# Optimization experiments

Measured on AMD Instinct MI355X. Metric: run time of the kernel, lower is better.

The kernel has to match this reference:

```python
import jax, jax.numpy as jnp
from jax import lax
import numpy as np

DECAY = 0.9
THRESH = 1.0


def setup_inputs() -> dict:
    key = jax.random.key(0)
    k1, k2, k3 = jax.random.split(key, 3)
    B, T, I, H, O = 64, 256, 1024, 2048, 1024
    x = jax.random.normal(k1, (B, T, I), dtype=jnp.float32)
    W1 = jax.random.normal(k2, (I, H), dtype=jnp.float32) * (1.0 / np.sqrt(I))
    b1 = jnp.zeros((H,), dtype=jnp.float32)
    W2 = jax.random.normal(k3, (H, O), dtype=jnp.float32) * (1.0 / np.sqrt(H))
    b2 = jnp.zeros((O,), dtype=jnp.float32)
    return {"x": x, "W1": W1, "b1": b1, "W2": W2, "b2": b2}


def reference(x, W1, b1, W2, b2):
    B, T, I = x.shape
    H = W1.shape[1]
    # Batch fc1 across all timesteps in one GEMM: [B,T,H]
    cur = jnp.einsum('bti,ih->bth', x, W1) + b1
    cur_tm = jnp.swapaxes(cur, 0, 1)  # [T,B,H] time-major for scan

    def step(carry, cur_t):
        mem, _ = carry
        mem = mem * DECAY + cur_t * (1.0 - DECAY)
        fired = mem > THRESH
        spk = jnp.where(fired, 1.0, 0.0).astype(mem.dtype)
        mem = jnp.where(fired, 0.0, mem)
        return (mem, spk), None

    mem0 = jnp.zeros((B, H), dtype=x.dtype)
    spk0 = jnp.zeros((B, H), dtype=x.dtype)
    (_, spk_last), _ = lax.scan(step, (mem0, spk0), cur_tm)
    # fc2 applied only to the final spike pattern, as in the original
    return spk_last @ W2 + b2
```

## Files before the change

### kernel.cpp

```cpp
#include <hip/hip_runtime.h>


typedef __attribute__((ext_vector_type(16))) float f32x16;
typedef __attribute__((ext_vector_type(8))) short s16x8;

#define GPTR(p) ((const __attribute__((address_space(1))) void*)(p))
#define SPTR(p) ((__attribute__((address_space(3))) void*)(p))

static constexpr int Bsz = 64, Tsz = 256, Isz = 1024, Hsz = 2048, Osz = 1024;
static constexpr int BK = 16;
static constexpr int NKT = Isz / BK;
static constexpr int NB = 128;
static constexpr int AL_OFF = 4096, B_OFF = 8192;
static constexpr int BUFEL = 12288;
static constexpr int ST = 68;
static constexpr int LDS_USHORTS = 3 * BUFEL;

__device__ __forceinline__ unsigned short f2bf(float f) {
  unsigned u = __float_as_uint(f);
  u += 0x7FFFu + ((u >> 16) & 1u);
  return (unsigned short)(u >> 16);
}
__device__ __forceinline__ float bf2f(unsigned short h) {
  return __uint_as_float(((unsigned)h) << 16);
}

__global__ void split_x_kernel(const float* __restrict__ x,
                               unsigned short* __restrict__ hi,
                               unsigned short* __restrict__ lo) {
  const long i = (long)blockIdx.x * 256 + threadIdx.x;
  const float4 v = ((const float4*)x)[i];
  const unsigned short hx = f2bf(v.x), hy = f2bf(v.y), hz = f2bf(v.z), hw = f2bf(v.w);
  ushort4 H, L;
  H.x = hx; H.y = hy; H.z = hz; H.w = hw;
  L.x = f2bf(v.x - bf2f(hx));
  L.y = f2bf(v.y - bf2f(hy));
  L.z = f2bf(v.z - bf2f(hz));
  L.w = f2bf(v.w - bf2f(hw));
  ((ushort4*)hi)[i] = H;
  ((ushort4*)lo)[i] = L;
}

__global__ void w1_transpose_split_kernel(const float* __restrict__ W1,
                                          unsigned short* __restrict__ wh,
                                          unsigned short* __restrict__ wl) {
  __shared__ float tile[32][33];
  const int h0 = blockIdx.x * 32;
  const int i0 = blockIdx.y * 32;
  const int c = threadIdx.x & 31;
  const int r4 = threadIdx.x >> 5;
#pragma unroll
  for (int s = 0; s < 4; ++s) {
    const int r = r4 + s * 8;
    tile[r][c] = W1[(long)(i0 + r) * Hsz + h0 + c];
  }
  __syncthreads();
#pragma unroll
  for (int s = 0; s < 4; ++s) {
    const int hr = r4 + s * 8;
    const float v = tile[c][hr];
    const unsigned short hh = f2bf(v);
    wh[(long)(h0 + hr) * Isz + i0 + c] = hh;
    wl[(long)(h0 + hr) * Isz + i0 + c] = f2bf(v - bf2f(hh));
  }
}

__global__ __launch_bounds__(512, 4) void gemm1_scan_kernel(
    const unsigned short* __restrict__ xh, const unsigned short* __restrict__ xl,
    const unsigned short* __restrict__ wth, const unsigned short* __restrict__ wtl,
    const float* __restrict__ b1, float* __restrict__ spk) {
  __shared__ __align__(16) unsigned short lds[LDS_USHORTS];

  const int tid = threadIdx.x;
  const int l = tid & 63;
  const int w = tid >> 6;
  const int wm = w >> 1;
  const int wn = w & 1;
  const int b = blockIdx.y;
  const int hb = blockIdx.x * NB;

  const int arow = tid >> 1;
  const int brow = (tid >> 1) & 127;
  const int ch8 = (tid & 1) * 8;
  const unsigned short* gAh = xh + (long)(b * Tsz + arow) * Isz + ch8;
  const unsigned short* gAl = xl + (long)(b * Tsz + arow) * Isz + ch8;
  const unsigned short* gB = ((tid < 256) ? wth : wtl) + (long)(hb + brow) * Isz + ch8;

#define STG(Q, KT) do {                                                                   \
    unsigned short* d_ = lds + (Q) * BUFEL + tid * 8;                                     \
    __builtin_amdgcn_global_load_lds(GPTR(gAh + (long)(KT) * BK), SPTR(d_), 16, 0, 0);    \
    __builtin_amdgcn_global_load_lds(GPTR(gAl + (long)(KT) * BK), SPTR(d_ + AL_OFF), 16, 0, 0); \
    __builtin_amdgcn_global_load_lds(GPTR(gB + (long)(KT) * BK), SPTR(d_ + B_OFF), 16, 0, 0);   \
  } while (0)

  const int lr = l & 31;
  const int kc = (l >> 5) * 8;
  const int aoff0 = (wm * 64 + lr) * 16 + kc;
  const int boff0 = B_OFF + (wn * 64 + lr) * 16 + kc;

  f32x16 acc[2][2];
#pragma unroll
  for (int i = 0; i < 2; ++i)
#pragma unroll
    for (int j = 0; j < 2; ++j) acc[i][j] = (f32x16)(0.f);

#define MM(MI, NI, AF, BF) \
  acc[MI][NI] = __builtin_amdgcn_mfma_f32_32x32x16_bf16(AF, BF, acc[MI][NI], 0, 0, 0)

  STG(0, 0);
  STG(1, 1);
  asm volatile("s_waitcnt vmcnt(3)" ::: "memory");
  __builtin_amdgcn_s_barrier();

  for (int kt = 0; kt < NKT; ++kt) {
    const int q = kt % 3;
    const unsigned short* p = lds + q * BUFEL;

    if (kt + 2 < NKT) {
      const int qn = (q >= 1) ? q - 1 : 2;
      STG(qn, kt + 2);
    }

    s16x8 Ah0 = *(const s16x8*)(p + aoff0);
    s16x8 Ah1 = *(const s16x8*)(p + aoff0 + 512);
    s16x8 Al0 = *(const s16x8*)(p + AL_OFF + aoff0);
    s16x8 Al1 = *(const s16x8*)(p + AL_OFF + aoff0 + 512);
    s16x8 Bh0 = *(const s16x8*)(p + boff0);
    s16x8 Bh1 = *(const s16x8*)(p + boff0 + 512);
    s16x8 Bl0 = *(const s16x8*)(p + boff0 + 2048);
    s16x8 Bl1 = *(const s16x8*)(p + boff0 + 2048 + 512);

    MM(0, 0, Ah0, Bh0); MM(0, 1, Ah0, Bh1);
    MM(1, 0, Ah1, Bh0); MM(1, 1, Ah1, Bh1);
    MM(0, 0, Ah0, Bl0); MM(0, 1, Ah0, Bl1);
    MM(1, 0, Ah1, Bl0); MM(1, 1, Ah1, Bl1);
    MM(0, 0, Al0, Bh0); MM(0, 1, Al0, Bh1);
    MM(1, 0, Al1, Bh0); MM(1, 1, Al1, Bh1);

    if (kt < NKT - 2) asm volatile("s_waitcnt vmcnt(3)" ::: "memory");
    else              asm volatile("s_waitcnt vmcnt(0)" ::: "memory");
    __builtin_amdgcn_s_barrier();
  }

  __syncthreads();
  float* scanbuf = reinterpret_cast<float*>(lds);
  float memv = 0.f;
  int fired = 0;
  const float b1v = (tid < NB) ? b1[hb + tid] : 0.f;

  for (int rnd = 0; rnd < 4; ++rnd) {
    if (wm == rnd) {
#pragma unroll
      for (int mi = 0; mi < 2; ++mi)
#pragma unroll
        for (int ni = 0; ni < 2; ++ni) {
          const int col = wn * 64 + ni * 32 + lr;
          float* dst = scanbuf + col * ST + mi * 32 + 4 * (l >> 5);
#pragma unroll
          for (int rq = 0; rq < 4; ++rq) {
            float4 v;
            v.x = acc[mi][ni][rq * 4 + 0];
            v.y = acc[mi][ni][rq * 4 + 1];
            v.z = acc[mi][ni][rq * 4 + 2];
            v.w = acc[mi][ni][rq * 4 + 3];
            *reinterpret_cast<float4*>(dst + 8 * rq) = v;
          }
        }
    }
    __syncthreads();
    if (tid < NB) {
      const float* src = scanbuf + tid * ST;
      float4 cur = *reinterpret_cast<const float4*>(src);
      for (int t0 = 0; t0 < 64; t0 += 4) {
        const int tn = (t0 + 4 < 64) ? t0 + 4 : t0;
        const float4 nxt = *reinterpret_cast<const float4*>(src + tn);
        float c;
        c = cur.x + b1v; memv = memv * 0.9f + c * 0.1f; fired = memv > 1.0f; if (fired) memv = 0.f;
        c = cur.y + b1v; memv = memv * 0.9f + c * 0.1f; fired = memv > 1.0f; if (fired) memv = 0.f;
        c = cur.z + b1v; memv = memv * 0.9f + c * 0.1f; fired = memv > 1.0f; if (fired) memv = 0.f;
        c = cur.w + b1v; memv = memv * 0.9f + c * 0.1f; fired = memv > 1.0f; if (fired) memv = 0.f;
        cur = nxt;
      }
    }
    __syncthreads();
  }
  if (tid < NB) spk[(long)b * Hsz + hb + tid] = fired ? 1.0f : 0.0f;
}

__global__ void gemm2_kernel(const float* __restrict__ spk, const float* __restrict__ W2,
                             const float* __restrict__ b2, float* __restrict__ out) {
  __shared__ int s_cnt[256];
  __shared__ int s_off[257];
  __shared__ int s_list[Hsz];
  const int b = blockIdx.x;
  const int tid = threadIdx.x;
  int hs[8];
  int c = 0;
#pragma unroll
  for (int e = 0; e < 8; ++e) {
    const int h = tid * 8 + e;
    if (spk[(long)b * Hsz + h] > 0.5f) hs[c++] = h;
  }
  s_cnt[tid] = c;
  __syncthreads();
  if (tid == 0) {
    int s = 0;
    for (int i = 0; i < 256; ++i) { s_off[i] = s; s += s_cnt[i]; }
    s_off[256] = s;
  }
  __syncthreads();
  {
    const int base = s_off[tid];
    for (int i = 0; i < c; ++i) s_list[base + i] = hs[i];
  }
  __syncthreads();
  const int total = s_off[256];
#pragma unroll
  for (int q = 0; q < 4; ++q) {
    const int o = q * 256 + tid;
    float v = b2[o];
    for (int i = 0; i < total; ++i) v += W2[(long)s_list[i] * Osz + o];
    out[(long)b * Osz + o] = v;
  }
}

extern "C" void kernel_launch(void* const* d_in, const int* in_sizes, int n_in,
                              void* d_out, int out_size, void* d_ws, size_t ws_size,
                              hipStream_t stream) {
  const float* x = (const float*)d_in[0];
  const float* W1 = (const float*)d_in[1];
  const float* b1 = (const float*)d_in[2];
  const float* W2 = (const float*)d_in[3];
  const float* b2 = (const float*)d_in[4];
  float* out = (float*)d_out;

  unsigned short* xh = (unsigned short*)d_ws;
  unsigned short* xl = xh + (long)Bsz * Tsz * Isz;
  unsigned short* wh = xl + (long)Bsz * Tsz * Isz;
  unsigned short* wl = wh + (long)Hsz * Isz;
  float* spk = (float*)(wl + (long)Hsz * Isz);

  split_x_kernel<<<(Bsz * Tsz * Isz) / (256 * 4), 256, 0, stream>>>(x, xh, xl);
  w1_transpose_split_kernel<<<dim3(Hsz / 32, Isz / 32), 256, 0, stream>>>(W1, wh, wl);
  gemm1_scan_kernel<<<dim3(Hsz / NB, Bsz), 512, 0, stream>>>(xh, xl, wh, wl, b1, spk);
  gemm2_kernel<<<Bsz, 256, 0, stream>>>(spk, W2, b2, out);
}
```

Measured before the change: 252.1 us.

## Enlarge per-wave GEMM tile to 128x64 with 256-thread blocks

Halves the block to 4 waves and gives each wave a 128x64 output tile (4x2 MFMA accumulators) instead of 64x64. Each B fragment read from LDS now feeds twice as many MFMAs, which cuts LDS read traffic per flop. Staging issues six global-to-LDS loads per thread to cover the same tile, and the wait counts are adjusted to match. The scan now runs in two rounds of 128 timesteps with a wider row stride. The price is more accumulator registers per wave and fewer resident waves to hide latency.

```diff
diff --git a/kernel.cpp b/kernel.cpp
--- a/kernel.cpp
+++ b/kernel.cpp
@@ -11,9 +11,9 @@
 static constexpr int BK = 16;
 static constexpr int NKT = Isz / BK;
 static constexpr int NB = 128;
-static constexpr int AL_OFF = 4096, B_OFF = 8192;
+static constexpr int AL_OFF = 4096, BH_OFF = 8192, BL_OFF = 10240;
 static constexpr int BUFEL = 12288;
-static constexpr int ST = 68;
+static constexpr int ST = 132;
 static constexpr int LDS_USHORTS = 3 * BUFEL;
 
 __device__ __forceinline__ unsigned short f2bf(float f) {
@@ -65,7 +65,7 @@
   }
 }
 
-__global__ __launch_bounds__(512, 4) void gemm1_scan_kernel(
+__global__ __launch_bounds__(256, 2) void gemm1_scan_kernel(
     const unsigned short* __restrict__ xh, const unsigned short* __restrict__ xl,
     const unsigned short* __restrict__ wth, const unsigned short* __restrict__ wtl,
     const float* __restrict__ b1, float* __restrict__ spk) {
@@ -79,28 +79,31 @@
   const int b = blockIdx.y;
   const int hb = blockIdx.x * NB;
 
-  const int arow = tid >> 1;
-  const int brow = (tid >> 1) & 127;
+  const int srow = tid >> 1;
   const int ch8 = (tid & 1) * 8;
-  const unsigned short* gAh = xh + (long)(b * Tsz + arow) * Isz + ch8;
-  const unsigned short* gAl = xl + (long)(b * Tsz + arow) * Isz + ch8;
-  const unsigned short* gB = ((tid < 256) ? wth : wtl) + (long)(hb + brow) * Isz + ch8;
+  const unsigned short* gAh = xh + (long)(b * Tsz + srow) * Isz + ch8;
+  const unsigned short* gAl = xl + (long)(b * Tsz + srow) * Isz + ch8;
+  const unsigned short* gBh = wth + (long)(hb + srow) * Isz + ch8;
+  const unsigned short* gBl = wtl + (long)(hb + srow) * Isz + ch8;
 
 #define STG(Q, KT) do {                                                                   \
     unsigned short* d_ = lds + (Q) * BUFEL + tid * 8;                                     \
     __builtin_amdgcn_global_load_lds(GPTR(gAh + (long)(KT) * BK), SPTR(d_), 16, 0, 0);    \
-    __builtin_amdgcn_global_load_lds(GPTR(gAl + (long)(KT) * BK), SPTR(d_ + AL_OFF), 16, 0, 0); \
-    __builtin_amdgcn_global_load_lds(GPTR(gB + (long)(KT) * BK), SPTR(d_ + B_OFF), 16, 0, 0);   \
+    __builtin_amdgcn_global_load_lds(GPTR(gAh + 128 * Isz + (long)(KT) * BK), SPTR(d_ + 2048), 16, 0, 0); \
+    __builtin_amdgcn_global_load_lds(GPTR(gAl + (long)(KT) * BK), SPTR(d_ + AL_OFF), 16, 0, 0);           \
+    __builtin_amdgcn_global_load_lds(GPTR(gAl + 128 * Isz + (long)(KT) * BK), SPTR(d_ + AL_OFF + 2048), 16, 0, 0); \
+    __builtin_amdgcn_global_load_lds(GPTR(gBh + (long)(KT) * BK), SPTR(d_ + BH_OFF), 16, 0, 0);           \
+    __builtin_amdgcn_global_load_lds(GPTR(gBl + (long)(KT) * BK), SPTR(d_ + BL_OFF), 16, 0, 0);           \
   } while (0)
 
   const int lr = l & 31;
   const int kc = (l >> 5) * 8;
-  const int aoff0 = (wm * 64 + lr) * 16 + kc;
-  const int boff0 = B_OFF + (wn * 64 + lr) * 16 + kc;
-
-  f32x16 acc[2][2];
-#pragma unroll
-  for (int i = 0; i < 2; ++i)
+  const int aoff = (wm * 128 + lr) * 16 + kc;
+  const int boff = BH_OFF + (wn * 64 + lr) * 16 + kc;
+
+  f32x16 acc[4][2];
+#pragma unroll
+  for (int i = 0; i < 4; ++i)
 #pragma unroll
     for (int j = 0; j < 2; ++j) acc[i][j] = (f32x16)(0.f);
 
@@ -109,7 +112,7 @@
 
   STG(0, 0);
   STG(1, 1);
-  asm volatile("s_waitcnt vmcnt(3)" ::: "memory");
+  asm volatile("s_waitcnt vmcnt(6)" ::: "memory");
   __builtin_amdgcn_s_barrier();
 
   for (int kt = 0; kt < NKT; ++kt) {
@@ -121,23 +124,33 @@
       STG(qn, kt + 2);
     }
 
-    s16x8 Ah0 = *(const s16x8*)(p + aoff0);
-    s16x8 Ah1 = *(const s16x8*)(p + aoff0 + 512);
-    s16x8 Al0 = *(const s16x8*)(p + AL_OFF + aoff0);
-    s16x8 Al1 = *(const s16x8*)(p + AL_OFF + aoff0 + 512);
-    s16x8 Bh0 = *(const s16x8*)(p + boff0);
-    s16x8 Bh1 = *(const s16x8*)(p + boff0 + 512);
-    s16x8 Bl0 = *(const s16x8*)(p + boff0 + 2048);
-    s16x8 Bl1 = *(const s16x8*)(p + boff0 + 2048 + 512);
+    s16x8 Ah0 = *(const s16x8*)(p + aoff);
+    s16x8 Ah1 = *(const s16x8*)(p + aoff + 512);
+    s16x8 Ah2 = *(const s16x8*)(p + aoff + 1024);
+    s16x8 Ah3 = *(const s16x8*)(p + aoff + 1536);
+    s16x8 Al0 = *(const s16x8*)(p + AL_OFF + aoff);
+    s16x8 Al1 = *(const s16x8*)(p + AL_OFF + aoff + 512);
+    s16x8 Al2 = *(const s16x8*)(p + AL_OFF + aoff + 1024);
+    s16x8 Al3 = *(const s16x8*)(p + AL_OFF + aoff + 1536);
+    s16x8 Bh0 = *(const s16x8*)(p + boff);
+    s16x8 Bh1 = *(const s16x8*)(p + boff + 512);
+    s16x8 Bl0 = *(const s16x8*)(p + boff + 2048);
+    s16x8 Bl1 = *(const s16x8*)(p + boff + 2048 + 512);
 
     MM(0, 0, Ah0, Bh0); MM(0, 1, Ah0, Bh1);
     MM(1, 0, Ah1, Bh0); MM(1, 1, Ah1, Bh1);
+    MM(2, 0, Ah2, Bh0); MM(2, 1, Ah2, Bh1);
+    MM(3, 0, Ah3, Bh0); MM(3, 1, Ah3, Bh1);
     MM(0, 0, Ah0, Bl0); MM(0, 1, Ah0, Bl1);
     MM(1, 0, Ah1, Bl0); MM(1, 1, Ah1, Bl1);
+    MM(2, 0, Ah2, Bl0); MM(2, 1, Ah2, Bl1);
+    MM(3, 0, Ah3, Bl0); MM(3, 1, Ah3, Bl1);
     MM(0, 0, Al0, Bh0); MM(0, 1, Al0, Bh1);
     MM(1, 0, Al1, Bh0); MM(1, 1, Al1, Bh1);
-
-    if (kt < NKT - 2) asm volatile("s_waitcnt vmcnt(3)" ::: "memory");
+    MM(2, 0, Al2, Bh0); MM(2, 1, Al2, Bh1);
+    MM(3, 0, Al3, Bh0); MM(3, 1, Al3, Bh1);
+
+    if (kt < NKT - 2) asm volatile("s_waitcnt vmcnt(6)" ::: "memory");
     else              asm volatile("s_waitcnt vmcnt(0)" ::: "memory");
     __builtin_amdgcn_s_barrier();
   }
@@ -148,10 +161,10 @@
   int fired = 0;
   const float b1v = (tid < NB) ? b1[hb + tid] : 0.f;
 
-  for (int rnd = 0; rnd < 4; ++rnd) {
+  for (int rnd = 0; rnd < 2; ++rnd) {
     if (wm == rnd) {
 #pragma unroll
-      for (int mi = 0; mi < 2; ++mi)
+      for (int mi = 0; mi < 4; ++mi)
 #pragma unroll
         for (int ni = 0; ni < 2; ++ni) {
           const int col = wn * 64 + ni * 32 + lr;
@@ -171,8 +184,8 @@
     if (tid < NB) {
       const float* src = scanbuf + tid * ST;
       float4 cur = *reinterpret_cast<const float4*>(src);
-      for (int t0 = 0; t0 < 64; t0 += 4) {
-        const int tn = (t0 + 4 < 64) ? t0 + 4 : t0;
+      for (int t0 = 0; t0 < 128; t0 += 4) {
+        const int tn = (t0 + 4 < 128) ? t0 + 4 : t0;
         const float4 nxt = *reinterpret_cast<const float4*>(src + tn);
         float c;
         c = cur.x + b1v; memv = memv * 0.9f + c * 0.1f; fired = memv > 1.0f; if (fired) memv = 0.f;
@@ -242,6 +255,6 @@
 
   split_x_kernel<<<(Bsz * Tsz * Isz) / (256 * 4), 256, 0, stream>>>(x, xh, xl);
   w1_transpose_split_kernel<<<dim3(Hsz / 32, Isz / 32), 256, 0, stream>>>(W1, wh, wl);
-  gemm1_scan_kernel<<<dim3(Hsz / NB, Bsz), 512, 0, stream>>>(xh, xl, wh, wl, b1, spk);
+  gemm1_scan_kernel<<<dim3(Hsz / NB, Bsz), 256, 0, stream>>>(xh, xl, wh, wl, b1, spk);
   gemm2_kernel<<<Bsz, 256, 0, stream>>>(spk, W2, b2, out);
 }
```

New measurement: 250.3 us. About the same (-0.7%).
